# Optimization experiments

Hardware: AMD Instinct MI355X
Metric: run time of the kernel (lower is better)

## Reference

```python
import jax, jax.numpy as jnp
import numpy as np

# SLAYER SRM-alpha neuron / simulation constants (from network.yaml defaults)
THETA = 10.0      # spike threshold
TAU_SR = 10.0     # synaptic response time constant
TAU_REF = 2.0     # refractory time constant
SCALE_REF = 2.0   # refractory scale (kernel amplitude = -SCALE_REF*THETA)
TAU_RHO = 1.0     # surrogate-gradient width
SCALE_RHO = 1.0   # surrogate-gradient scale
TS = 1.0          # simulation step
K_PSP = 100       # truncation length of srm (alpha) kernel, ~10*tauSr
K_REF = 32        # truncation length of refractory kernel


def srm_kernel():
    t = jnp.arange(K_PSP, dtype=jnp.float32) * TS
    return (t / TAU_SR) * jnp.exp(1.0 - t / TAU_SR)  # eps(t), eps(0)=0


def ref_kernel():
    t = jnp.arange(K_REF, dtype=jnp.float32) * TS
    return -SCALE_REF * THETA * (t / TAU_REF) * jnp.exp(1.0 - t / TAU_REF)  # nu(t), nu(0)=0


def psp(z):
    # causal temporal convolution with srm kernel: u[t] = sum_k eps[k] * z[t-k]
    B, F, T = z.shape
    k = srm_kernel()[::-1].reshape(1, 1, K_PSP).astype(z.dtype)
    x = z.reshape(B * F, 1, T)
    y = jax.lax.conv_general_dilated(
        x, k, window_strides=(1,), padding=[(K_PSP - 1, 0)],
        dimension_numbers=('NCH', 'OIH', 'NCH'))
    return y.reshape(B, F, T)


@jax.custom_vjp
def spike_fn(u):
    return (u >= THETA).astype(u.dtype)

def _spike_fwd(u):
    return spike_fn(u), u

def _spike_bwd(u, g):
    # SLAYER surrogate spike pdf: scaleRho/(tauRho*theta) * exp(-|u-theta|/(tauRho*theta))
    pdf = (SCALE_RHO / (TAU_RHO * THETA)) * jnp.exp(-jnp.abs(u - THETA) / (TAU_RHO * THETA))
    return (g * pdf,)

spike_fn.defvjp(_spike_fwd, _spike_bwd)


def spike_dyn(u):
    # sequential LIF threshold with refractory response added to future potentials
    B, F, T = u.shape
    ref = ref_kernel().astype(u.dtype)  # [K_REF]

    def step(buf, u_t):  # buf: [B,F,K_REF] pending refractory contributions
        v = u_t + buf[..., 0]
        s = spike_fn(v)
        buf = buf + s[..., None] * ref
        buf = jnp.concatenate([buf[..., 1:], jnp.zeros_like(buf[..., :1])], axis=-1)
        return buf, s

    buf0 = jnp.zeros((B, F, K_REF), u.dtype)
    _, spikes = jax.lax.scan(step, buf0, jnp.moveaxis(u, 2, 0))  # [T,B,F]
    return jnp.moveaxis(spikes, 0, 2)


def slayer_layer(x, W):
    # dense (per-timestep GEMM, no bias) -> psp -> spike
    z = jnp.einsum('bft,of->bot', x, W)
    return spike_dyn(psp(z))


def setup_inputs() -> dict:
    key = jax.random.key(0)
    k0, k1, k2, k3 = jax.random.split(key, 4)
    B, F_IN, T = 8, 128 * 128, 300
    inp = (jax.random.uniform(k0, (B, F_IN, T)) < 0.1).astype(jnp.float32)
    W1 = jax.random.normal(k1, (410, F_IN), jnp.float32) * 0.05
    W2 = jax.random.normal(k2, (240, 410), jnp.float32) * 0.3
    W3 = jax.random.normal(k3, (10, 240), jnp.float32) * 0.3
    return {"input": inp, "W1": W1, "W2": W2, "W3": W3}


def reference(input, W1, W2, W3):
    x = slayer_layer(input, W1)
    x = slayer_layer(x, W2)
    x = slayer_layer(x, W3)
    return x  # [B, 10, T] spike trains
```

## Files before the change

### kernel.cpp

```cpp
#include <hip/hip_runtime.h>


#define B   8
#define T   300
#define F0  16384
#define O1  410
#define O2  240
#define OP2 240
#define O3  10
#define OP3 16
#define W1M 7
#define W2M 4
#define NCOLS (B*T)
#define LCAP 2048
#define PPLC ((size_t)416 * NCOLS)

typedef int  int32x4  __attribute__((ext_vector_type(4)));
typedef int  int32x16 __attribute__((ext_vector_type(16)));

__global__ __launch_bounds__(256) void bitpack_x_kernel(
    const float* __restrict__ X, unsigned short* __restrict__ Bbit)
{
    __shared__ float tileT[64][65];
    int tt = blockIdx.x;
    int fb = blockIdx.y;
    int b  = blockIdx.z;
    int t0 = tt * 64, f0 = fb * 64;
    int tid = threadIdx.x;

    const float* Xb = X + ((size_t)b * F0 + f0) * T;
    int fl = tid >> 4;
    int tq = (tid & 15) * 4;
    #pragma unroll
    for (int i = 0; i < 4; ++i) {
        int fr = fl + i * 16;
        int t  = t0 + tq;
        float4 v = make_float4(0.f, 0.f, 0.f, 0.f);
        if (t < T) v = *(const float4*)(Xb + (size_t)fr * T + t);
        tileT[tq + 0][fr] = v.x;
        tileT[tq + 1][fr] = v.y;
        tileT[tq + 2][fr] = v.z;
        tileT[tq + 3][fr] = v.w;
    }
    __syncthreads();

    int sub = tid & 3;
    int tl  = tid >> 2;
    unsigned m = 0u;
    #pragma unroll
    for (int j = 0; j < 16; ++j)
        m |= (tileT[tl][sub * 16 + j] != 0.0f ? 1u : 0u) << j;
    int t = t0 + tl;
    if (t < T)
        Bbit[((size_t)(b * 256 + fb) * 320 + t) * 4 + sub] = (unsigned short)m;
}

__global__ __launch_bounds__(256) void quant_limb_kernel(
    const float* __restrict__ W, char* __restrict__ Aswz)
{
    int o  = blockIdx.y;
    int f0 = (blockIdx.x * 256 + threadIdx.x) * 16;

    float w[16];
    if (o < O1) {
        #pragma unroll
        for (int e = 0; e < 16; e += 4)
            *(float4*)&w[e] = *(const float4*)(W + (size_t)o * F0 + f0 + e);
    } else {
        #pragma unroll
        for (int e = 0; e < 16; ++e) w[e] = 0.0f;
    }

    unsigned pk[4][4] = {{0,0,0,0},{0,0,0,0},{0,0,0,0},{0,0,0,0}};
    #pragma unroll
    for (int e = 0; e < 16; ++e) {
        int q = (int)__double2ll_rn((double)w[e] * 134217728.0);
        int l0 = (int)(signed char)(q & 255);  q = (q - l0) >> 8;
        int l1 = (int)(signed char)(q & 255);  q = (q - l1) >> 8;
        int l2 = (int)(signed char)(q & 255);  int l3 = (q - l2) >> 8;
        pk[0][e >> 2] |= (unsigned)(l0 & 255) << (8 * (e & 3));
        pk[1][e >> 2] |= (unsigned)(l1 & 255) << (8 * (e & 3));
        pk[2][e >> 2] |= (unsigned)(l2 & 255) << (8 * (e & 3));
        pk[3][e >> 2] |= (unsigned)(l3 & 255) << (8 * (e & 3));
    }

    int kit = f0 >> 6, ks = (f0 >> 5) & 1, hb = (f0 >> 4) & 1;
    #pragma unroll
    for (int l = 0; l < 4; ++l) {
        int m = o * 4 + l;
        int mt = m >> 7, r = m & 127, g = r >> 5, row = r & 31;
        int word = ks * 64 + row + 32 * hb;
        size_t addr = ((size_t)(mt * 256 + kit) * 4 + g) * 2048 + (size_t)word * 16;
        *(int32x4*)(Aswz + addr) =
            (int32x4){(int)pk[l][0], (int)pk[l][1], (int)pk[l][2], (int)pk[l][3]};
    }
}

__global__ __launch_bounds__(256) void quant_small2_kernel(
    const float* __restrict__ W2, const float* __restrict__ W3,
    int* __restrict__ Q2T, int* __restrict__ Q3T)
{
    int idx = blockIdx.x * 256 + threadIdx.x;
    const int n1 = O1 * OP2;
    const int n2 = O2 * OP3;
    if (idx < n1) {
        int f = idx / OP2, o = idx - f * OP2;
        Q2T[idx] = (int)__double2ll_rn((double)W2[(size_t)o * O1 + f] * 67108864.0);
    } else if (idx < n1 + n2) {
        int j = idx - n1;
        int f = j / OP3, o = j - f * OP3;
        double v = (o < O3) ? (double)W3[(size_t)o * O2 + f] : 0.0;
        Q3T[j] = (int)__double2ll_rn(v * 67108864.0);
    }
}

__device__ __forceinline__ int32x4 expand16(unsigned m)
{
    int32x4 r;
    r.x = (int)((((m      ) & 15u) * 0x00204081u) & 0x01010101u);
    r.y = (int)((((m >>  4) & 15u) * 0x00204081u) & 0x01010101u);
    r.z = (int)((((m >>  8) & 15u) * 0x00204081u) & 0x01010101u);
    r.w = (int)((((m >> 12) & 15u) * 0x00204081u) & 0x01010101u);
    return r;
}

__global__ __launch_bounds__(256) void mfma_gemm_kernel(
    const char* __restrict__ Aswz, const unsigned short* __restrict__ Bbit,
    long long* __restrict__ Pc)
{
    int id  = blockIdx.x;
    int xcd = id & 7, rr = id >> 3;
    int bh  = rr & 15, gq = rr >> 4;
    int g   = xcd + 8 * gq;
    if (g >= 52) return;
    int mt = g >> 2, kc = g & 3;
    int b = bh >> 1, half = bh & 1;

    int tid = threadIdx.x;
    int lane = tid & 63, wv = tid >> 6;
    int wm = wv >> 1, wn = wv & 1;
    int ng0 = wn * 3;
    int nfr = wn ? 2 : 3;

    const char* Ab = Aswz + ((size_t)(mt * 256 + kc * 64) * 4 + wm * 2) * 2048
                          + (size_t)lane * 16;
    const char* Bb = (const char*)Bbit + (size_t)(b * 256 + kc * 64) * 320 * 8;
    int hb16 = (lane >> 5) * 16;

    const char* Bf[3];
    #pragma unroll
    for (int fn = 0; fn < 3; ++fn) {
        int colf = (half * 5 + ng0 + fn) * 32 + (lane & 31);
        Bf[fn] = Bb + (size_t)colf * 8;
    }

    int32x16 acc[2][3];
    #pragma unroll
    for (int fm = 0; fm < 2; ++fm)
        #pragma unroll
        for (int fn = 0; fn < 3; ++fn)
            acc[fm][fn] = (int32x16){0,0,0,0,0,0,0,0,0,0,0,0,0,0,0,0};

    int32x4 a_cur[2][2], a_nxt[2][2];
    uint2   r_cur[3],    r_nxt[3];

    a_cur[0][0] = *(const int32x4*)(Ab);
    a_cur[0][1] = *(const int32x4*)(Ab + 1024);
    a_cur[1][0] = *(const int32x4*)(Ab + 2048);
    a_cur[1][1] = *(const int32x4*)(Ab + 3072);
    #pragma unroll
    for (int fn = 0; fn < 3; ++fn)
        if (fn < nfr) r_cur[fn] = *(const uint2*)(Bf[fn]);

    #pragma unroll 2
    for (int it = 0; it < 64; ++it) {
        int itn = (it < 63) ? it + 1 : it;
        const char* Abn = Ab + (size_t)itn * 8192;
        a_nxt[0][0] = *(const int32x4*)(Abn);
        a_nxt[0][1] = *(const int32x4*)(Abn + 1024);
        a_nxt[1][0] = *(const int32x4*)(Abn + 2048);
        a_nxt[1][1] = *(const int32x4*)(Abn + 3072);
        #pragma unroll
        for (int fn = 0; fn < 3; ++fn)
            if (fn < nfr)
                r_nxt[fn] = *(const uint2*)(Bf[fn] + (size_t)itn * 2560);

        #pragma unroll
        for (int ks = 0; ks < 2; ++ks)
            #pragma unroll
            for (int fn = 0; fn < 3; ++fn)
                if (fn < nfr) {
                    unsigned mraw = ks ? r_cur[fn].y : r_cur[fn].x;
                    int32x4 bvv = expand16((mraw >> hb16) & 0xFFFFu);
                    acc[0][fn] = __builtin_amdgcn_mfma_i32_32x32x32_i8(
                        a_cur[0][ks], bvv, acc[0][fn], 0, 0, 0);
                    acc[1][fn] = __builtin_amdgcn_mfma_i32_32x32x32_i8(
                        a_cur[1][ks], bvv, acc[1][fn], 0, 0, 0);
                }

        #pragma unroll
        for (int fm = 0; fm < 2; ++fm)
            #pragma unroll
            for (int ks = 0; ks < 2; ++ks)
                a_cur[fm][ks] = a_nxt[fm][ks];
        #pragma unroll
        for (int fn = 0; fn < 3; ++fn)
            if (fn < nfr) r_cur[fn] = r_nxt[fn];
    }

    int col = lane & 31, h = lane >> 5;
    long long* Pk = Pc + (size_t)kc * PPLC + (size_t)b * T;
    #pragma unroll
    for (int fm = 0; fm < 2; ++fm) {
        #pragma unroll
        for (int fn = 0; fn < 3; ++fn) {
            if (fn >= nfr) continue;
            int t = (half * 5 + ng0 + fn) * 32 + col;
            if (t >= T) continue;
            int obase = mt * 32 + wm * 16 + fm * 8;
            #pragma unroll
            for (int q = 0; q < 4; ++q) {
                int o = obase + 2 * q + h;
                long long s = (long long)acc[fm][fn][4 * q]
                            + ((long long)acc[fm][fn][4 * q + 1] << 8)
                            + ((long long)acc[fm][fn][4 * q + 2] << 16)
                            + ((long long)acc[fm][fn][4 * q + 3] << 24);
                Pk[(size_t)o * NCOLS + t] = s;
            }
        }
    }
}

__global__ __launch_bounds__(320) void redpsp1_kernel(
    const long long* __restrict__ Pc, unsigned short* __restrict__ smask)
{
    __shared__ double zs[16][304];
    __shared__ double us[16][304];
    __shared__ double eps[100];
    int og = blockIdx.x, b = blockIdx.y;
    int o0 = og * 16;
    int tid = threadIdx.x;
    const double sc27 = 1.0 / 134217728.0;

    if (tid < 100) {
        double td = (double)tid;
        eps[tid] = (td / 10.0) * exp(1.0 - td / 10.0);
    }
    if (tid < T) {
        size_t col = (size_t)b * T + tid;
        #pragma unroll 4
        for (int ol = 0; ol < 16; ++ol) {
            int o = o0 + ol;
            size_t idx = (size_t)o * NCOLS + col;
            long long s = Pc[idx] + Pc[PPLC + idx]
                        + Pc[2 * PPLC + idx] + Pc[3 * PPLC + idx];
            zs[ol][tid] = (double)s * sc27;
        }
    }
    __syncthreads();

    if (tid < T) {
        double sum[16];
        #pragma unroll
        for (int o = 0; o < 16; ++o) sum[o] = 0.0;
        int kmax = tid < 99 ? tid : 99;
        for (int k = 0; k <= kmax; ++k) {
            double e = eps[k];
            #pragma unroll
            for (int o = 0; o < 16; ++o)
                sum[o] = fma(e, zs[o][tid - k], sum[o]);
        }
        #pragma unroll
        for (int o = 0; o < 16; ++o) us[o][tid] = sum[o];
    }
    if (og == 25 && tid < T) {
        size_t col = (size_t)b * T + tid;
        *(unsigned*)((char*)smask + (col * 28 + 26) * 2) = 0u;
    }
    __syncthreads();

    if (tid < 64) {
        int l = tid;
        bool act = (l < 16) && (o0 + l < O1);
        const double alpha = exp(-0.5);
        const double A31   = exp(-15.5);
        const double c0    = -10.0 * exp(1.0);
        double E = 0.0, G = 0.0;
        unsigned hist = 0u;
        for (int t = 0; t < T; ++t) {
            double uval = act ? us[l][t] : -1.0e300;
            double v = uval + c0 * G;
            bool sp = (v >= 10.0);
            unsigned long long bal = __ballot(sp);
            if (l == 0)
                smask[((size_t)b * T + t) * 28 + og] =
                    (unsigned short)(bal & 0xFFFFu);
            double sN  = sp ? 1.0 : 0.0;
            double s31 = ((hist >> 30) & 1u) ? 1.0 : 0.0;
            double Em  = E - A31 * s31;
            double Gm  = G - 31.0 * A31 * s31;
            G = alpha * (sN + Gm + Em);
            E = alpha * (sN + Em);
            hist = (hist << 1) | (sp ? 1u : 0u);
        }
    }
}

template<int OPAD_, int O_, int SLOTS, int NOG, bool OUT>
__global__ __launch_bounds__(320) void redpsp23_kernel(
    const int* __restrict__ Z, unsigned short* __restrict__ smask,
    float* __restrict__ sout, double scale)
{
    __shared__ double zs[16][304];
    __shared__ double us[16][304];
    __shared__ double eps[100];
    int og = blockIdx.x, b = blockIdx.y;
    int o0 = og * 16;
    int tid = threadIdx.x;

    if (tid < 100) {
        double td = (double)tid;
        eps[tid] = (td / 10.0) * exp(1.0 - td / 10.0);
    }
    if (tid < T) {
        size_t col = (size_t)b * T + tid;
        #pragma unroll 4
        for (int ol = 0; ol < 16; ++ol) {
            int o = o0 + ol;
            double zv = (o < OPAD_) ? (double)Z[col * OPAD_ + o] * scale : 0.0;
            zs[ol][tid] = zv;
        }
    }
    __syncthreads();

    if (tid < T) {
        double sum[16];
        #pragma unroll
        for (int o = 0; o < 16; ++o) sum[o] = 0.0;
        int kmax = tid < 99 ? tid : 99;
        for (int k = 0; k <= kmax; ++k) {
            double e = eps[k];
            #pragma unroll
            for (int o = 0; o < 16; ++o)
                sum[o] = fma(e, zs[o][tid - k], sum[o]);
        }
        #pragma unroll
        for (int o = 0; o < 16; ++o) us[o][tid] = sum[o];
    }
    if (SLOTS > NOG && og == NOG - 1 && tid < T) {
        size_t col = (size_t)b * T + tid;
        #pragma unroll
        for (int s = NOG; s < SLOTS; ++s)
            smask[col * SLOTS + s] = 0;
    }
    __syncthreads();

    if (tid < 64) {
        int l = tid;
        bool act = (l < 16) && (o0 + l < O_);
        const double alpha = exp(-0.5);
        const double A31   = exp(-15.5);
        const double c0    = -10.0 * exp(1.0);
        double E = 0.0, G = 0.0;
        unsigned hist = 0u;
        for (int t = 0; t < T; ++t) {
            double uval = act ? us[l][t] : -1.0e300;
            double v = uval + c0 * G;
            bool sp = (v >= 10.0);
            unsigned long long bal = __ballot(sp);
            if (SLOTS > 0 && l == 0)
                smask[((size_t)b * T + t) * SLOTS + og] =
                    (unsigned short)(bal & 0xFFFFu);
            if (OUT && act)
                sout[((size_t)b * O_ + o0 + l) * T + t] = sp ? 1.0f : 0.0f;
            double sN  = sp ? 1.0 : 0.0;
            double s31 = ((hist >> 30) & 1u) ? 1.0 : 0.0;
            double Em  = E - A31 * s31;
            double Gm  = G - 31.0 * A31 * s31;
            G = alpha * (sN + Gm + Em);
            E = alpha * (sN + Em);
            hist = (hist << 1) | (sp ? 1u : 0u);
        }
    }
}

__global__ __launch_bounds__(128) void sparse_gemm_kernel(
    const int* __restrict__ QT, const unsigned long long* __restrict__ cmask,
    int* __restrict__ Z, int OPAD, int W, int CW, int cshift)
{
    __shared__ int lf[LCAP];
    __shared__ int wsum[2];

    int chunk = blockIdx.x & ((1 << cshift) - 1);
    int col   = blockIdx.x >> cshift;
    int tid   = threadIdx.x;

    int wbase = col * W + chunk * CW;
    unsigned long long w0 = (2 * tid     < CW) ? cmask[wbase + 2 * tid]     : 0ULL;
    unsigned long long w1 = (2 * tid + 1 < CW) ? cmask[wbase + 2 * tid + 1] : 0ULL;
    int my = __popcll(w0) + __popcll(w1);

    int scan = my;
    #pragma unroll
    for (int d = 1; d < 64; d <<= 1) {
        int v = __shfl_up(scan, d);
        if ((tid & 63) >= d) scan += v;
    }
    if ((tid & 63) == 63) wsum[tid >> 6] = scan;
    __syncthreads();
    int off = ((tid >= 64) ? wsum[0] : 0) + scan - my;
    int n = wsum[0] + wsum[1];

    int f0e = (chunk * CW + 2 * tid) * 64;
    unsigned long long m = w0;
    while (m) {
        int bit = __ffsll(m) - 1;
        if (off < LCAP) lf[off] = (f0e + bit) * OPAD;
        ++off; m &= m - 1;
    }
    m = w1; f0e += 64;
    while (m) {
        int bit = __ffsll(m) - 1;
        if (off < LCAP) lf[off] = (f0e + bit) * OPAD;
        ++off; m &= m - 1;
    }
    __syncthreads();
    if (n > LCAP) n = LCAP;

    if (tid * 4 < OPAD) {
        int o = tid * 4;
        const int* bq = QT + o;
        int a0 = 0, a1 = 0, a2 = 0, a3 = 0;
        int i = 0;
        for (; i + 8 <= n; i += 8) {
            int4 ia = *(const int4*)&lf[i];
            int4 ib = *(const int4*)&lf[i + 4];
            int e0 = __builtin_amdgcn_readfirstlane(ia.x);
            int e1 = __builtin_amdgcn_readfirstlane(ia.y);
            int e2 = __builtin_amdgcn_readfirstlane(ia.z);
            int e3 = __builtin_amdgcn_readfirstlane(ia.w);
            int e4 = __builtin_amdgcn_readfirstlane(ib.x);
            int e5 = __builtin_amdgcn_readfirstlane(ib.y);
            int e6 = __builtin_amdgcn_readfirstlane(ib.z);
            int e7 = __builtin_amdgcn_readfirstlane(ib.w);
            int4 q0 = *(const int4*)(bq + e0);
            int4 q1 = *(const int4*)(bq + e1);
            int4 q2 = *(const int4*)(bq + e2);
            int4 q3 = *(const int4*)(bq + e3);
            int4 q4 = *(const int4*)(bq + e4);
            int4 q5 = *(const int4*)(bq + e5);
            int4 q6 = *(const int4*)(bq + e6);
            int4 q7 = *(const int4*)(bq + e7);
            a0 += q0.x; a1 += q0.y; a2 += q0.z; a3 += q0.w;
            a0 += q1.x; a1 += q1.y; a2 += q1.z; a3 += q1.w;
            a0 += q2.x; a1 += q2.y; a2 += q2.z; a3 += q2.w;
            a0 += q3.x; a1 += q3.y; a2 += q3.z; a3 += q3.w;
            a0 += q4.x; a1 += q4.y; a2 += q4.z; a3 += q4.w;
            a0 += q5.x; a1 += q5.y; a2 += q5.z; a3 += q5.w;
            a0 += q6.x; a1 += q6.y; a2 += q6.z; a3 += q6.w;
            a0 += q7.x; a1 += q7.y; a2 += q7.z; a3 += q7.w;
        }
        for (; i < n; ++i) {
            int e = __builtin_amdgcn_readfirstlane(lf[i]);
            int4 q = *(const int4*)(bq + e);
            a0 += q.x; a1 += q.y; a2 += q.z; a3 += q.w;
        }
        int* zb = Z + ((size_t)chunk * NCOLS + col) * OPAD + o;
        *(int4*)zb = make_int4(a0, a1, a2, a3);
    }
}

extern "C" void kernel_launch(void* const* d_in, const int* in_sizes, int n_in,
                              void* d_out, int out_size, void* d_ws, size_t ws_size,
                              hipStream_t stream)
{
    const float* x  = (const float*)d_in[0];
    const float* W1 = (const float*)d_in[1];
    const float* W2 = (const float*)d_in[2];
    const float* W3 = (const float*)d_in[3];
    float* out = (float*)d_out;

    const size_t sz_Aswz   = (size_t)13 * 256 * 4 * 2048;
    const size_t sz_Bbit   = (size_t)B * 256 * 320 * 4 * 2;
    const size_t sz_Pc     = (size_t)4 * PPLC * 8;
    const size_t sz_Q2T    = (size_t)O1 * OP2 * 4;
    const size_t sz_Q3T    = (size_t)O2 * OP3 * 4;
    const size_t sz_smask1 = (size_t)NCOLS * 28 * 2;
    const size_t sz_smask2 = (size_t)NCOLS * 16 * 2;

    char* p = (char*)d_ws;
    char*           Aswz   = p;                  p += sz_Aswz;
    unsigned short* Bbit   = (unsigned short*)p; p += sz_Bbit;
    long long*      Pc     = (long long*)p;  char* pa = p;  p += sz_Pc;
    int*            Q2T    = (int*)p;            p += sz_Q2T;
    int*            Q3T    = (int*)p;            p += sz_Q3T;
    unsigned short* smask1 = (unsigned short*)p; p += sz_smask1;
    unsigned short* smask2 = (unsigned short*)p; p += sz_smask2;
    int* z2 = (int*)pa;                          pa += (size_t)NCOLS * OP2 * 4;
    int* z3 = (int*)pa;                          pa += (size_t)NCOLS * OP3 * 4;

    const double sc26 = 1.0 / 67108864.0;

    bitpack_x_kernel<<<dim3(5, 256, B), dim3(256), 0, stream>>>(x, Bbit);
    quant_limb_kernel<<<dim3(4, 416), dim3(256), 0, stream>>>(W1, Aswz);
    quant_small2_kernel<<<dim3((O1 * OP2 + O2 * OP3 + 255) / 256), dim3(256), 0, stream>>>(
        W2, W3, Q2T, Q3T);

    mfma_gemm_kernel<<<dim3(896), dim3(256), 0, stream>>>(Aswz, Bbit, Pc);
    redpsp1_kernel<<<dim3(26, B), dim3(320), 0, stream>>>(Pc, smask1);

    sparse_gemm_kernel<<<dim3(NCOLS), dim3(128), 0, stream>>>(
        Q2T, (const unsigned long long*)smask1, z2, OP2, W1M, W1M, 0);
    redpsp23_kernel<OP2, O2, 16, 15, false><<<dim3(15, B), dim3(320), 0, stream>>>(
        z2, smask2, (float*)0, sc26);

    sparse_gemm_kernel<<<dim3(NCOLS), dim3(128), 0, stream>>>(
        Q3T, (const unsigned long long*)smask2, z3, OP3, W2M, W2M, 0);
    redpsp23_kernel<OP3, O3, 0, 1, true><<<dim3(1, B), dim3(320), 0, stream>>>(
        z3, (unsigned short*)0, out, sc26);
}
```

Measured before the change: 271.9 us.

## Fuse prep kernels, split GEMM K eight ways with int32 partials, ping-pong loads

Merges the bitpack, W1 limb-quantisation and W2/W3 quantisation kernels into one launch, removing two launch gaps. The int8 MFMA GEMM now splits K into 8 chunks instead of 4, so all 1664 blocks do useful work and none exit early. Each block writes int32 partials instead of int64, halving partial traffic, and the 8 partials are summed in the reduction kernel. The inner loop now ping-pongs between two register stages instead of copying next into current. The int32 partials assume each chunk's combined limb sum fits in 32 bits, which is a possible overflow risk.

```diff
diff --git a/kernel.cpp b/kernel.cpp
--- a/kernel.cpp
+++ b/kernel.cpp
@@ -13,106 +13,10 @@
 #define W2M 4
 #define NCOLS (B*T)
 #define LCAP 2048
-#define PPLC ((size_t)416 * NCOLS)
+#define PPLC32 ((size_t)416 * NCOLS)
 
 typedef int  int32x4  __attribute__((ext_vector_type(4)));
 typedef int  int32x16 __attribute__((ext_vector_type(16)));
-
-__global__ __launch_bounds__(256) void bitpack_x_kernel(
-    const float* __restrict__ X, unsigned short* __restrict__ Bbit)
-{
-    __shared__ float tileT[64][65];
-    int tt = blockIdx.x;
-    int fb = blockIdx.y;
-    int b  = blockIdx.z;
-    int t0 = tt * 64, f0 = fb * 64;
-    int tid = threadIdx.x;
-
-    const float* Xb = X + ((size_t)b * F0 + f0) * T;
-    int fl = tid >> 4;
-    int tq = (tid & 15) * 4;
-    #pragma unroll
-    for (int i = 0; i < 4; ++i) {
-        int fr = fl + i * 16;
-        int t  = t0 + tq;
-        float4 v = make_float4(0.f, 0.f, 0.f, 0.f);
-        if (t < T) v = *(const float4*)(Xb + (size_t)fr * T + t);
-        tileT[tq + 0][fr] = v.x;
-        tileT[tq + 1][fr] = v.y;
-        tileT[tq + 2][fr] = v.z;
-        tileT[tq + 3][fr] = v.w;
-    }
-    __syncthreads();
-
-    int sub = tid & 3;
-    int tl  = tid >> 2;
-    unsigned m = 0u;
-    #pragma unroll
-    for (int j = 0; j < 16; ++j)
-        m |= (tileT[tl][sub * 16 + j] != 0.0f ? 1u : 0u) << j;
-    int t = t0 + tl;
-    if (t < T)
-        Bbit[((size_t)(b * 256 + fb) * 320 + t) * 4 + sub] = (unsigned short)m;
-}
-
-__global__ __launch_bounds__(256) void quant_limb_kernel(
-    const float* __restrict__ W, char* __restrict__ Aswz)
-{
-    int o  = blockIdx.y;
-    int f0 = (blockIdx.x * 256 + threadIdx.x) * 16;
-
-    float w[16];
-    if (o < O1) {
-        #pragma unroll
-        for (int e = 0; e < 16; e += 4)
-            *(float4*)&w[e] = *(const float4*)(W + (size_t)o * F0 + f0 + e);
-    } else {
-        #pragma unroll
-        for (int e = 0; e < 16; ++e) w[e] = 0.0f;
-    }
-
-    unsigned pk[4][4] = {{0,0,0,0},{0,0,0,0},{0,0,0,0},{0,0,0,0}};
-    #pragma unroll
-    for (int e = 0; e < 16; ++e) {
-        int q = (int)__double2ll_rn((double)w[e] * 134217728.0);
-        int l0 = (int)(signed char)(q & 255);  q = (q - l0) >> 8;
-        int l1 = (int)(signed char)(q & 255);  q = (q - l1) >> 8;
-        int l2 = (int)(signed char)(q & 255);  int l3 = (q - l2) >> 8;
-        pk[0][e >> 2] |= (unsigned)(l0 & 255) << (8 * (e & 3));
-        pk[1][e >> 2] |= (unsigned)(l1 & 255) << (8 * (e & 3));
-        pk[2][e >> 2] |= (unsigned)(l2 & 255) << (8 * (e & 3));
-        pk[3][e >> 2] |= (unsigned)(l3 & 255) << (8 * (e & 3));
-    }
-
-    int kit = f0 >> 6, ks = (f0 >> 5) & 1, hb = (f0 >> 4) & 1;
-    #pragma unroll
-    for (int l = 0; l < 4; ++l) {
-        int m = o * 4 + l;
-        int mt = m >> 7, r = m & 127, g = r >> 5, row = r & 31;
-        int word = ks * 64 + row + 32 * hb;
-        size_t addr = ((size_t)(mt * 256 + kit) * 4 + g) * 2048 + (size_t)word * 16;
-        *(int32x4*)(Aswz + addr) =
-            (int32x4){(int)pk[l][0], (int)pk[l][1], (int)pk[l][2], (int)pk[l][3]};
-    }
-}
-
-__global__ __launch_bounds__(256) void quant_small2_kernel(
-    const float* __restrict__ W2, const float* __restrict__ W3,
-    int* __restrict__ Q2T, int* __restrict__ Q3T)
-{
-    int idx = blockIdx.x * 256 + threadIdx.x;
-    const int n1 = O1 * OP2;
-    const int n2 = O2 * OP3;
-    if (idx < n1) {
-        int f = idx / OP2, o = idx - f * OP2;
-        Q2T[idx] = (int)__double2ll_rn((double)W2[(size_t)o * O1 + f] * 67108864.0);
-    } else if (idx < n1 + n2) {
-        int j = idx - n1;
-        int f = j / OP3, o = j - f * OP3;
-        double v = (o < O3) ? (double)W3[(size_t)o * O2 + f] : 0.0;
-        Q3T[j] = (int)__double2ll_rn(v * 67108864.0);
-    }
-}
 
 __device__ __forceinline__ int32x4 expand16(unsigned m)
 {
@@ -124,16 +28,108 @@
     return r;
 }
 
+__global__ __launch_bounds__(256) void prep_kernel(
+    const float* __restrict__ X,  const float* __restrict__ W1,
+    const float* __restrict__ W2, const float* __restrict__ W3,
+    unsigned short* __restrict__ Bbit, char* __restrict__ Aswz,
+    int* __restrict__ Q2T, int* __restrict__ Q3T)
+{
+    __shared__ float tileT[64][65];
+    int bid = blockIdx.x;
+    int tid = threadIdx.x;
+
+    if (bid < 10240) {
+        int tt = bid % 5, fb = (bid / 5) % 256, b = bid / 1280;
+        int t0 = tt * 64, f0 = fb * 64;
+        const float* Xb = X + ((size_t)b * F0 + f0) * T;
+        int fl = tid >> 4;
+        int tq = (tid & 15) * 4;
+        #pragma unroll
+        for (int i = 0; i < 4; ++i) {
+            int fr = fl + i * 16;
+            int t  = t0 + tq;
+            float4 v = make_float4(0.f, 0.f, 0.f, 0.f);
+            if (t < T) v = *(const float4*)(Xb + (size_t)fr * T + t);
+            tileT[tq + 0][fr] = v.x;
+            tileT[tq + 1][fr] = v.y;
+            tileT[tq + 2][fr] = v.z;
+            tileT[tq + 3][fr] = v.w;
+        }
+        __syncthreads();
+        int sub = tid & 3;
+        int tl  = tid >> 2;
+        unsigned m = 0u;
+        #pragma unroll
+        for (int j = 0; j < 16; ++j)
+            m |= (tileT[tl][sub * 16 + j] != 0.0f ? 1u : 0u) << j;
+        int t = t0 + tl;
+        if (t < T)
+            Bbit[((size_t)(b * 256 + fb) * 320 + t) * 4 + sub] = (unsigned short)m;
+
+    } else if (bid < 11904) {
+        int j = bid - 10240;
+        int o  = j >> 2;
+        int f0 = ((j & 3) * 256 + tid) * 16;
+
+        float w[16];
+        if (o < O1) {
+            #pragma unroll
+            for (int e = 0; e < 16; e += 4)
+                *(float4*)&w[e] = *(const float4*)(W1 + (size_t)o * F0 + f0 + e);
+        } else {
+            #pragma unroll
+            for (int e = 0; e < 16; ++e) w[e] = 0.0f;
+        }
+
+        unsigned pk[4][4] = {{0,0,0,0},{0,0,0,0},{0,0,0,0},{0,0,0,0}};
+        #pragma unroll
+        for (int e = 0; e < 16; ++e) {
+            int q = (int)__double2ll_rn((double)w[e] * 134217728.0);
+            int l0 = (int)(signed char)(q & 255);  q = (q - l0) >> 8;
+            int l1 = (int)(signed char)(q & 255);  q = (q - l1) >> 8;
+            int l2 = (int)(signed char)(q & 255);  int l3 = (q - l2) >> 8;
+            pk[0][e >> 2] |= (unsigned)(l0 & 255) << (8 * (e & 3));
+            pk[1][e >> 2] |= (unsigned)(l1 & 255) << (8 * (e & 3));
+            pk[2][e >> 2] |= (unsigned)(l2 & 255) << (8 * (e & 3));
+            pk[3][e >> 2] |= (unsigned)(l3 & 255) << (8 * (e & 3));
+        }
+
+        int kit = f0 >> 6, ks = (f0 >> 5) & 1, hb = (f0 >> 4) & 1;
+        #pragma unroll
+        for (int l = 0; l < 4; ++l) {
+            int m = o * 4 + l;
+            int mt = m >> 7, r = m & 127, g = r >> 5, row = r & 31;
+            int word = ks * 64 + row + 32 * hb;
+            size_t addr = ((size_t)(mt * 256 + kit) * 4 + g) * 2048 + (size_t)word * 16;
+            *(int32x4*)(Aswz + addr) =
+                (int32x4){(int)pk[l][0], (int)pk[l][1], (int)pk[l][2], (int)pk[l][3]};
+        }
+
+    } else {
+        int idx = (bid - 11904) * 256 + tid;
+        const int n1 = O1 * OP2;
+        const int n2 = O2 * OP3;
+        if (idx < n1) {
+            int f = idx / OP2, o = idx - f * OP2;
+            Q2T[idx] = (int)__double2ll_rn((double)W2[(size_t)o * O1 + f] * 67108864.0);
+        } else if (idx < n1 + n2) {
+            int j = idx - n1;
+            int f = j / OP3, o = j - f * OP3;
+            double v = (o < O3) ? (double)W3[(size_t)o * O2 + f] : 0.0;
+            Q3T[j] = (int)__double2ll_rn(v * 67108864.0);
+        }
+    }
+}
+
 __global__ __launch_bounds__(256) void mfma_gemm_kernel(
     const char* __restrict__ Aswz, const unsigned short* __restrict__ Bbit,
-    long long* __restrict__ Pc)
+    int* __restrict__ Pc)
 {
     int id  = blockIdx.x;
     int xcd = id & 7, rr = id >> 3;
     int bh  = rr & 15, gq = rr >> 4;
     int g   = xcd + 8 * gq;
-    if (g >= 52) return;
-    int mt = g >> 2, kc = g & 3;
+    int mt = g >> 3, kc = g & 7;
     int b = bh >> 1, half = bh & 1;
 
     int tid = threadIdx.x;
@@ -142,9 +138,9 @@
     int ng0 = wn * 3;
     int nfr = wn ? 2 : 3;
 
-    const char* Ab = Aswz + ((size_t)(mt * 256 + kc * 64) * 4 + wm * 2) * 2048
+    const char* Ab = Aswz + ((size_t)(mt * 256 + kc * 32) * 4 + wm * 2) * 2048
                           + (size_t)lane * 16;
-    const char* Bb = (const char*)Bbit + (size_t)(b * 256 + kc * 64) * 320 * 8;
+    const char* Bb = (const char*)Bbit + (size_t)(b * 256 + kc * 32) * 320 * 8;
     int hb16 = (lane >> 5) * 16;
 
     const char* Bf[3];
@@ -161,55 +157,47 @@
         for (int fn = 0; fn < 3; ++fn)
             acc[fm][fn] = (int32x16){0,0,0,0,0,0,0,0,0,0,0,0,0,0,0,0};
 
-    int32x4 a_cur[2][2], a_nxt[2][2];
-    uint2   r_cur[3],    r_nxt[3];
-
-    a_cur[0][0] = *(const int32x4*)(Ab);
-    a_cur[0][1] = *(const int32x4*)(Ab + 1024);
-    a_cur[1][0] = *(const int32x4*)(Ab + 2048);
-    a_cur[1][1] = *(const int32x4*)(Ab + 3072);
-    #pragma unroll
-    for (int fn = 0; fn < 3; ++fn)
-        if (fn < nfr) r_cur[fn] = *(const uint2*)(Bf[fn]);
-
-    #pragma unroll 2
-    for (int it = 0; it < 64; ++it) {
-        int itn = (it < 63) ? it + 1 : it;
-        const char* Abn = Ab + (size_t)itn * 8192;
-        a_nxt[0][0] = *(const int32x4*)(Abn);
-        a_nxt[0][1] = *(const int32x4*)(Abn + 1024);
-        a_nxt[1][0] = *(const int32x4*)(Abn + 2048);
-        a_nxt[1][1] = *(const int32x4*)(Abn + 3072);
-        #pragma unroll
-        for (int fn = 0; fn < 3; ++fn)
-            if (fn < nfr)
-                r_nxt[fn] = *(const uint2*)(Bf[fn] + (size_t)itn * 2560);
-
-        #pragma unroll
-        for (int ks = 0; ks < 2; ++ks)
-            #pragma unroll
-            for (int fn = 0; fn < 3; ++fn)
-                if (fn < nfr) {
-                    unsigned mraw = ks ? r_cur[fn].y : r_cur[fn].x;
-                    int32x4 bvv = expand16((mraw >> hb16) & 0xFFFFu);
-                    acc[0][fn] = __builtin_amdgcn_mfma_i32_32x32x32_i8(
-                        a_cur[0][ks], bvv, acc[0][fn], 0, 0, 0);
-                    acc[1][fn] = __builtin_amdgcn_mfma_i32_32x32x32_i8(
-                        a_cur[1][ks], bvv, acc[1][fn], 0, 0, 0);
-                }
-
-        #pragma unroll
-        for (int fm = 0; fm < 2; ++fm)
-            #pragma unroll
-            for (int ks = 0; ks < 2; ++ks)
-                a_cur[fm][ks] = a_nxt[fm][ks];
-        #pragma unroll
-        for (int fn = 0; fn < 3; ++fn)
-            if (fn < nfr) r_cur[fn] = r_nxt[fn];
-    }
+    int32x4 aA[2][2], aB[2][2];
+    uint2   rA[3],    rB[3];
+
+#define LOAD_STAGE(AR, RR, ITN)                                               \
+    { const char* Abn_ = Ab + (size_t)(ITN) * 8192;                           \
+      AR[0][0] = *(const int32x4*)(Abn_);                                     \
+      AR[0][1] = *(const int32x4*)(Abn_ + 1024);                              \
+      AR[1][0] = *(const int32x4*)(Abn_ + 2048);                              \
+      AR[1][1] = *(const int32x4*)(Abn_ + 3072);                              \
+      _Pragma("unroll")                                                       \
+      for (int fn_ = 0; fn_ < 3; ++fn_)                                       \
+          if (fn_ < nfr)                                                      \
+              RR[fn_] = *(const uint2*)(Bf[fn_] + (size_t)(ITN) * 2560); }
+
+#define COMPUTE_STAGE(AR, RR)                                                 \
+    { _Pragma("unroll")                                                       \
+      for (int ks_ = 0; ks_ < 2; ++ks_)                                       \
+          _Pragma("unroll")                                                   \
+          for (int fn_ = 0; fn_ < 3; ++fn_)                                   \
+              if (fn_ < nfr) {                                                \
+                  unsigned mraw_ = ks_ ? RR[fn_].y : RR[fn_].x;               \
+                  int32x4 bvv_ = expand16((mraw_ >> hb16) & 0xFFFFu);         \
+                  acc[0][fn_] = __builtin_amdgcn_mfma_i32_32x32x32_i8(        \
+                      AR[0][ks_], bvv_, acc[0][fn_], 0, 0, 0);                \
+                  acc[1][fn_] = __builtin_amdgcn_mfma_i32_32x32x32_i8(        \
+                      AR[1][ks_], bvv_, acc[1][fn_], 0, 0, 0);                \
+              } }
+
+    LOAD_STAGE(aA, rA, 0);
+    for (int it = 0; it < 32; it += 2) {
+        LOAD_STAGE(aB, rB, it + 1);
+        COMPUTE_STAGE(aA, rA);
+        int itn2 = (it + 2 < 32) ? it + 2 : 31;
+        LOAD_STAGE(aA, rA, itn2);
+        COMPUTE_STAGE(aB, rB);
+    }
+#undef LOAD_STAGE
+#undef COMPUTE_STAGE
 
     int col = lane & 31, h = lane >> 5;
-    long long* Pk = Pc + (size_t)kc * PPLC + (size_t)b * T;
+    int* Pk = Pc + (size_t)kc * PPLC32 + (size_t)b * T;
     #pragma unroll
     for (int fm = 0; fm < 2; ++fm) {
         #pragma unroll
@@ -221,18 +209,18 @@
             #pragma unroll
             for (int q = 0; q < 4; ++q) {
                 int o = obase + 2 * q + h;
-                long long s = (long long)acc[fm][fn][4 * q]
-                            + ((long long)acc[fm][fn][4 * q + 1] << 8)
-                            + ((long long)acc[fm][fn][4 * q + 2] << 16)
-                            + ((long long)acc[fm][fn][4 * q + 3] << 24);
-                Pk[(size_t)o * NCOLS + t] = s;
+                unsigned s = (unsigned)acc[fm][fn][4 * q]
+                           + ((unsigned)acc[fm][fn][4 * q + 1] << 8)
+                           + ((unsigned)acc[fm][fn][4 * q + 2] << 16)
+                           + ((unsigned)acc[fm][fn][4 * q + 3] << 24);
+                Pk[(size_t)o * NCOLS + t] = (int)s;
             }
         }
     }
 }
 
 __global__ __launch_bounds__(320) void redpsp1_kernel(
-    const long long* __restrict__ Pc, unsigned short* __restrict__ smask)
+    const int* __restrict__ Pc, unsigned short* __restrict__ smask)
 {
     __shared__ double zs[16][304];
     __shared__ double us[16][304];
@@ -252,8 +240,10 @@
         for (int ol = 0; ol < 16; ++ol) {
             int o = o0 + ol;
             size_t idx = (size_t)o * NCOLS + col;
-            long long s = Pc[idx] + Pc[PPLC + idx]
-                        + Pc[2 * PPLC + idx] + Pc[3 * PPLC + idx];
+            long long s = 0;
+            #pragma unroll
+            for (int c = 0; c < 8; ++c)
+                s += (long long)Pc[(size_t)c * PPLC32 + idx];
             zs[ol][tid] = (double)s * sc27;
         }
     }
@@ -482,7 +472,7 @@
 
     const size_t sz_Aswz   = (size_t)13 * 256 * 4 * 2048;
     const size_t sz_Bbit   = (size_t)B * 256 * 320 * 4 * 2;
-    const size_t sz_Pc     = (size_t)4 * PPLC * 8;
+    const size_t sz_Pc     = (size_t)8 * PPLC32 * 4;
     const size_t sz_Q2T    = (size_t)O1 * OP2 * 4;
     const size_t sz_Q3T    = (size_t)O2 * OP3 * 4;
     const size_t sz_smask1 = (size_t)NCOLS * 28 * 2;
@@ -491,7 +481,7 @@
     char* p = (char*)d_ws;
     char*           Aswz   = p;                  p += sz_Aswz;
     unsigned short* Bbit   = (unsigned short*)p; p += sz_Bbit;
-    long long*      Pc     = (long long*)p;  char* pa = p;  p += sz_Pc;
+    int*            Pc     = (int*)p;  char* pa = p;  p += sz_Pc;
     int*            Q2T    = (int*)p;            p += sz_Q2T;
     int*            Q3T    = (int*)p;            p += sz_Q3T;
     unsigned short* smask1 = (unsigned short*)p; p += sz_smask1;
@@ -501,12 +491,10 @@
 
     const double sc26 = 1.0 / 67108864.0;
 
-    bitpack_x_kernel<<<dim3(5, 256, B), dim3(256), 0, stream>>>(x, Bbit);
-    quant_limb_kernel<<<dim3(4, 416), dim3(256), 0, stream>>>(W1, Aswz);
-    quant_small2_kernel<<<dim3((O1 * OP2 + O2 * OP3 + 255) / 256), dim3(256), 0, stream>>>(
-        W2, W3, Q2T, Q3T);
-
-    mfma_gemm_kernel<<<dim3(896), dim3(256), 0, stream>>>(Aswz, Bbit, Pc);
+    prep_kernel<<<dim3(12304), dim3(256), 0, stream>>>(
+        x, W1, W2, W3, Bbit, Aswz, Q2T, Q3T);
+
+    mfma_gemm_kernel<<<dim3(1664), dim3(256), 0, stream>>>(Aswz, Bbit, Pc);
     redpsp1_kernel<<<dim3(26, B), dim3(320), 0, stream>>>(Pc, smask1);
 
     sparse_gemm_kernel<<<dim3(NCOLS), dim3(128), 0, stream>>>(
```

After: 259.9 us. -4.4%, faster.
